# Performance work log

Hardware: AMD Instinct MI355X
Metric: run time of the kernel (lower is better)

## Reference

```python
import jax, jax.numpy as jnp
import numpy as np

IN_F = 4096
OUT_F = 4096
N_VALS = 4096
N_TOKENS = 4096


def setup_inputs() -> dict:
    key = jax.random.key(0)
    k_x, k_v, k_i = jax.random.split(key, 3)
    x = jax.random.normal(k_x, (N_TOKENS, IN_F), dtype=jnp.float32)
    # codebook of memristor conductance differences (sorted, as in load_values)
    values = jnp.sort(jax.random.normal(k_v, (N_VALS,), dtype=jnp.float32))
    w_idx = jax.random.randint(k_i, (OUT_F, IN_F), 0, N_VALS, dtype=jnp.int64)
    bias = jnp.zeros((OUT_F,), dtype=jnp.float32)
    return {"x": x, "values": values, "w_idx": w_idx, "bias": bias}


def reference(x, values, w_idx, bias):
    # dequantize weight from codebook: (out_f, in_f)
    weight = values[w_idx]
    # F.linear(x, weight, bias) == x @ weight.T + bias
    return jnp.einsum("ti,oi->to", x, weight) + bias
```

## Files before the change

### kernel.cpp

```cpp
#include <hip/hip_runtime.h>
#include <hip/hip_bf16.h>
#include <stdint.h>

typedef unsigned short u16;
typedef __bf16 bf16x8 __attribute__((ext_vector_type(8)));
typedef float  f32x4  __attribute__((ext_vector_type(4)));
typedef u16    u16x8  __attribute__((ext_vector_type(8)));
typedef u16    u16x4  __attribute__((ext_vector_type(4)));

__device__ __forceinline__ u16 f2bf(float f) {
  union { float f; unsigned u; } v; v.f = f;
  unsigned u = v.u;
  unsigned r = u + 0x7FFFu + ((u >> 16) & 1u);
  return (u16)(r >> 16);
}

__device__ __forceinline__ void gld_lds16(const void* g, void* l) {
  __builtin_amdgcn_global_load_lds(
      (const __attribute__((address_space(1))) void*)g,
      (__attribute__((address_space(3))) void*)l, 16, 0, 0);
}

__global__ void detect_idx_width(const unsigned* __restrict__ w, int* __restrict__ flag) {
  unsigned v = w[threadIdx.x * 2 + 1];
  unsigned long long any = __ballot(v != 0u);
  if (threadIdx.x == 0) *flag = (any != 0ull) ? 1 : 0;
}

__global__ __launch_bounds__(256) void cvt_x_kernel(const float4* __restrict__ x,
                                                    u16* __restrict__ xb, long n8) {
  long i = (long)blockIdx.x * blockDim.x + threadIdx.x;
  long stride = (long)gridDim.x * blockDim.x;
  for (; i < n8; i += stride) {
    float4 a = x[2 * i];
    float4 b = x[2 * i + 1];
    u16x8 r;
    r[0] = f2bf(a.x); r[1] = f2bf(a.y); r[2] = f2bf(a.z); r[3] = f2bf(a.w);
    r[4] = f2bf(b.x); r[5] = f2bf(b.y); r[6] = f2bf(b.z); r[7] = f2bf(b.w);
    *(u16x8*)(xb + 8 * i) = r;
  }
}

__global__ __launch_bounds__(256) void dequant_w_kernel(const int4* __restrict__ widx,
                                                        const float* __restrict__ values,
                                                        u16* __restrict__ wb,
                                                        const int* __restrict__ flag, long n4) {
  const bool is32 = (*flag != 0);
  long i = (long)blockIdx.x * blockDim.x + threadIdx.x;
  long stride = (long)gridDim.x * blockDim.x;
  for (; i < n4; i += stride) {
    int i0, i1, i2, i3;
    if (is32) {
      int4 v = widx[i];
      i0 = v.x; i1 = v.y; i2 = v.z; i3 = v.w;
    } else {
      int4 a = widx[2 * i];
      int4 b = widx[2 * i + 1];
      i0 = a.x; i1 = a.z; i2 = b.x; i3 = b.z;
    }
    u16x4 r;
    r[0] = f2bf(values[i0]); r[1] = f2bf(values[i1]);
    r[2] = f2bf(values[i2]); r[3] = f2bf(values[i3]);
    *(u16x4*)(wb + 4 * i) = r;
  }
}

#define VMW(n) asm volatile("s_waitcnt vmcnt(" #n ")" ::: "memory")
#define SB0    __builtin_amdgcn_sched_barrier(0)
#define PH_BAR __builtin_amdgcn_s_barrier()

__global__ __launch_bounds__(512, 1) void gemm256_kernel(
    const u16* __restrict__ Xb, const u16* __restrict__ Wb,
    const float* __restrict__ bias, float* __restrict__ C,
    int Nout, int Kin) {
  __shared__ __align__(16) char lds[163840];

  const int tid  = threadIdx.x;
  const int lane = tid & 63;
  const int wave = tid >> 6;
  const int wr = wave >> 2;
  const int wc = wave & 3;

  const int nwg = gridDim.x;
  const int bid = blockIdx.x;
  const int q8 = nwg >> 3, r8 = nwg & 7;
  const int xcd = bid & 7;
  const int wg = (xcd < r8 ? xcd * (q8 + 1) : r8 * (q8 + 1) + (xcd - r8) * q8) + (bid >> 3);

  const int tiles_n = Nout / 256;
  const long brow = (long)(wg / tiles_n) * 256;
  const long bcol = (long)(wg % tiles_n) * 256;

  const long rowb = (long)Kin * 2;
  const long rstep = 64 * rowb;
  const long hstep = 128 * rowb;

  const int f0  = tid * 16;
  const int f1  = f0 + 8192;
  const int rS0 = f0 >> 7;
  const int cS  = (f0 & 127) ^ ((rS0 & 7) << 4);
  const int voff = (int)(rS0 * rowb) + cS;

  const char* uA = (const char*)Xb + (size_t)brow * rowb;
  const char* uB = (const char*)Wb + (size_t)bcol * rowb;

#define STAGE_AH(base_, h, t) { \
  gld_lds16(uA + (size_t)(h) * hstep + (size_t)(t) * 128 + voff,         lds + (base_) + (h) * 16384 + f0); \
  gld_lds16(uA + (size_t)(h) * hstep + (size_t)(t) * 128 + rstep + voff, lds + (base_) + (h) * 16384 + f1); }
#define STAGE_BH(base_, h, t) { \
  gld_lds16(uB + (size_t)(h) * hstep + (size_t)(t) * 128 + voff,         lds + (base_) + (h) * 16384 + f0); \
  gld_lds16(uB + (size_t)(h) * hstep + (size_t)(t) * 128 + rstep + voff, lds + (base_) + (h) * 16384 + f1); }

  const int fr   = lane & 15;
  const int kb   = (lane >> 4) * 16;
  const int xsw  = (fr & 7) << 4;
  const int colx0 = kb ^ xsw;
  const int colx1 = (64 + kb) ^ xsw;
  const int aOff = wr * 16384 + fr * 128;
  const int bOff = (wc >> 1) * 16384 + ((wc & 1) * 64 + fr) * 128;

  bf16x8 afr0[2][2];
  bf16x8 afr1[2][2];
  bf16x8 bfrE[4][2];
  bf16x8 bfrO[4][2];
  f32x4  acc[8][4] = {};

#define READ_AQ(abase_, q, DST) { \
  const char* ab = lds + (abase_) + aOff + (q) * 4096; \
  DST[0][0] = *(const bf16x8*)(ab + colx0); \
  DST[0][1] = *(const bf16x8*)(ab + colx1); \
  DST[1][0] = *(const bf16x8*)(ab + 2048 + colx0); \
  DST[1][1] = *(const bf16x8*)(ab + 2048 + colx1); }

#define READ_BPF(bbase_, dst, lo) { \
  const char* bb = lds + (bbase_) + bOff; \
  dst[(lo)][0]     = *(const bf16x8*)(bb + (lo) * 2048 + colx0); \
  dst[(lo)][1]     = *(const bf16x8*)(bb + (lo) * 2048 + colx1); \
  dst[(lo) + 1][0] = *(const bf16x8*)(bb + ((lo) + 1) * 2048 + colx0); \
  dst[(lo) + 1][1] = *(const bf16x8*)(bb + ((lo) + 1) * 2048 + colx1); }

#define MFMA_Q(q, AF, BF) { \
  __builtin_amdgcn_s_setprio(1); \
  _Pragma("unroll") for (int m2 = 0; m2 < 2; ++m2) \
  _Pragma("unroll") for (int ni = 0; ni < 4; ++ni) { \
    acc[(q)*2+m2][ni] = __builtin_amdgcn_mfma_f32_16x16x32_bf16(AF[m2][0], BF[ni][0], acc[(q)*2+m2][ni], 0, 0, 0); \
    acc[(q)*2+m2][ni] = __builtin_amdgcn_mfma_f32_16x16x32_bf16(AF[m2][1], BF[ni][1], acc[(q)*2+m2][ni], 0, 0, 0); } \
  __builtin_amdgcn_s_setprio(0); }

#define PHASE(RDS, STG, MF, WT) { \
  RDS; STG; SB0; PH_BAR; SB0; MF; SB0; WT; PH_BAR; }

  const int aB0 = 0, aB1 = 32768;
  int bR0 = 65536, bR1 = 98304, bR2 = 131072;
  const int NT = Kin >> 6;

  STAGE_AH(aB0, 0, 0); STAGE_AH(aB0, 1, 0);
  STAGE_BH(bR0, 0, 0); STAGE_BH(bR0, 1, 0);
  if (NT > 1) { STAGE_BH(bR1, 0, 1); STAGE_BH(bR1, 1, 1); }
  if (NT > 2) { STAGE_BH(bR2, 0, 2); STAGE_BH(bR2, 1, 2); }
  VMW(0);
  PH_BAR;
  READ_BPF(bR0, bfrE, 0); READ_BPF(bR0, bfrE, 2);
  READ_AQ(aB0, 0, afr0);

  const int NITER = NT >> 1;
  for (int i = 0; i < NITER; ++i) {
    const int t0 = i * 2;
    const bool a1 = (t0 + 1 < NT);
    const bool a2 = (t0 + 2 < NT);
    const bool b3 = (t0 + 3 < NT);
    const bool b4 = (t0 + 4 < NT);

    PHASE(READ_AQ(aB0, 1, afr1),
          { if (a1) STAGE_AH(aB1, 0, t0 + 1); },
          MFMA_Q(0, afr0, bfrE), (void)0);
    PHASE({ READ_AQ(aB0, 2, afr0); READ_BPF(bR1, bfrO, 0); },
          { if (a1) STAGE_AH(aB1, 1, t0 + 1); },
          MFMA_Q(1, afr1, bfrE), (void)0);
    PHASE({ READ_AQ(aB0, 3, afr1); READ_BPF(bR1, bfrO, 2); },
          { if (b3) STAGE_BH(bR0, 0, t0 + 3); },
          MFMA_Q(2, afr0, bfrE),
          { if (b3) { VMW(2); } else { VMW(0); } });
    PHASE({ if (a1) READ_AQ(aB1, 0, afr0); },
          { if (b3) STAGE_BH(bR0, 1, t0 + 3); },
          MFMA_Q(3, afr1, bfrE), (void)0);

    PHASE(READ_AQ(aB1, 1, afr1),
          { if (a2) STAGE_AH(aB0, 0, t0 + 2); },
          MFMA_Q(0, afr0, bfrO), (void)0);
    PHASE({ READ_AQ(aB1, 2, afr0); if (a2) READ_BPF(bR2, bfrE, 0); },
          { if (a2) STAGE_AH(aB0, 1, t0 + 2); },
          MFMA_Q(1, afr1, bfrO), (void)0);
    PHASE({ READ_AQ(aB1, 3, afr1); if (a2) READ_BPF(bR2, bfrE, 2); },
          { if (b4) STAGE_BH(bR1, 0, t0 + 4); },
          MFMA_Q(2, afr0, bfrO),
          { if (b4) { VMW(2); } else { VMW(0); } });
    PHASE({ if (a2) READ_AQ(aB0, 0, afr0); },
          { if (b4) STAGE_BH(bR1, 1, t0 + 4); },
          MFMA_Q(3, afr1, bfrO), (void)0);

    int tmp = bR0; bR0 = bR2; bR2 = bR1; bR1 = tmp;
  }

  const int cm = (lane >> 4) * 4;
  const int cn = lane & 15;
  float bv[4];
#pragma unroll
  for (int ni = 0; ni < 4; ++ni) bv[ni] = bias[bcol + wc * 64 + ni * 16 + cn];

#pragma unroll
  for (int mi = 0; mi < 8; ++mi) {
    const long row0 = brow + wr * 128 + mi * 16 + cm;
#pragma unroll
    for (int ni = 0; ni < 4; ++ni) {
      const long col = bcol + wc * 64 + ni * 16 + cn;
#pragma unroll
      for (int j = 0; j < 4; ++j)
        C[(row0 + j) * (long)Nout + col] = acc[mi][ni][j] + bv[ni];
    }
  }
#undef STAGE_AH
#undef STAGE_BH
#undef READ_AQ
#undef READ_BPF
#undef MFMA_Q
#undef PHASE
}

__global__ __launch_bounds__(256, 2) void gemm128_kernel(
    const u16* __restrict__ Xb, const u16* __restrict__ Wb,
    const float* __restrict__ bias, float* __restrict__ C,
    int Nout, int Kin) {
  __shared__ __align__(16) u16 As[128 * 32];
  __shared__ __align__(16) u16 Bs[128 * 32];
  const int tid  = threadIdx.x;
  const int lane = tid & 63;
  const int wave = tid >> 6;
  const int wr = wave >> 1, wc = wave & 1;
  const int nwg = gridDim.x, bid = blockIdx.x;
  const int q = nwg >> 3, r8 = nwg & 7;
  const int xcd = bid & 7;
  const int wg = (xcd < r8 ? xcd * (q + 1) : r8 * (q + 1) + (xcd - r8) * q) + (bid >> 3);
  const int tiles_n = Nout / 128;
  const long brow = (long)(wg / tiles_n) * 128;
  const long bcol = (long)(wg % tiles_n) * 128;
  const int f0 = tid * 16, f1 = f0 + 4096;
  const size_t rowbytes = (size_t)Kin * 2;
  const char* gA0 = (const char*)Xb + (size_t)(brow + (f0 >> 6)) * rowbytes + (f0 & 63);
  const char* gA1 = (const char*)Xb + (size_t)(brow + (f1 >> 6)) * rowbytes + (f1 & 63);
  const char* gB0 = (const char*)Wb + (size_t)(bcol + (f0 >> 6)) * rowbytes + (f0 & 63);
  const char* gB1 = (const char*)Wb + (size_t)(bcol + (f1 >> 6)) * rowbytes + (f1 & 63);
  char* lA0 = (char*)As + f0; char* lA1 = (char*)As + f1;
  char* lB0 = (char*)Bs + f0; char* lB1 = (char*)Bs + f1;
  const int fr = lane & 15, kb = (lane >> 4) * 16;
  const char* aptr[4]; const char* bptr[4];
#pragma unroll
  for (int i = 0; i < 4; ++i) {
    aptr[i] = (const char*)As + (wr * 64 + i * 16 + fr) * 64 + kb;
    bptr[i] = (const char*)Bs + (wc * 64 + i * 16 + fr) * 64 + kb;
  }
  f32x4 acc[4][4] = {};
  for (int kk = 0; kk < Kin; kk += 32) {
    const size_t ko = (size_t)kk * 2;
    gld_lds16(gA0 + ko, lA0); gld_lds16(gA1 + ko, lA1);
    gld_lds16(gB0 + ko, lB0); gld_lds16(gB1 + ko, lB1);
    __syncthreads();
    bf16x8 a[4], b[4];
#pragma unroll
    for (int i = 0; i < 4; ++i) a[i] = *(const bf16x8*)aptr[i];
#pragma unroll
    for (int i = 0; i < 4; ++i) b[i] = *(const bf16x8*)bptr[i];
#pragma unroll
    for (int mi = 0; mi < 4; ++mi)
#pragma unroll
      for (int ni = 0; ni < 4; ++ni)
        acc[mi][ni] = __builtin_amdgcn_mfma_f32_16x16x32_bf16(a[mi], b[ni], acc[mi][ni], 0, 0, 0);
    __syncthreads();
  }
  const int cm = (lane >> 4) * 4, cn = lane & 15;
  float bv[4];
#pragma unroll
  for (int ni = 0; ni < 4; ++ni) bv[ni] = bias[bcol + wc * 64 + ni * 16 + cn];
#pragma unroll
  for (int mi = 0; mi < 4; ++mi) {
    const long row0 = brow + wr * 64 + mi * 16 + cm;
#pragma unroll
    for (int ni = 0; ni < 4; ++ni) {
      const long col = bcol + wc * 64 + ni * 16 + cn;
#pragma unroll
      for (int j = 0; j < 4; ++j)
        C[(row0 + j) * (long)Nout + col] = acc[mi][ni][j] + bv[ni];
    }
  }
}

__global__ void fallback_kernel(const float* __restrict__ x, const float* __restrict__ values,
                                const int* __restrict__ widx, const float* __restrict__ bias,
                                float* __restrict__ out, const int* __restrict__ flag,
                                int NT, int IF, int OF) {
  const int o = blockIdx.x * blockDim.x + threadIdx.x;
  const int t = blockIdx.y;
  if (o >= OF || t >= NT) return;
  const bool is32 = (*flag != 0);
  const float* xr = x + (size_t)t * IF;
  float sum = 0.f;
  if (is32) {
    const int* w = widx + (size_t)o * IF;
    for (int k = 0; k < IF; ++k) sum += xr[k] * values[w[k]];
  } else {
    const long long* w = (const long long*)widx + (size_t)o * IF;
    for (int k = 0; k < IF; ++k) sum += xr[k] * values[(int)w[k]];
  }
  out[(size_t)t * OF + o] = sum + bias[o];
}

extern "C" void kernel_launch(void* const* d_in, const int* in_sizes, int n_in,
                              void* d_out, int out_size, void* d_ws, size_t ws_size,
                              hipStream_t stream) {
  const float* x      = (const float*)d_in[0];
  const float* values = (const float*)d_in[1];
  const int*   widx   = (const int*)d_in[2];
  const float* bias   = (const float*)d_in[3];
  float* out = (float*)d_out;

  const long xsz = in_sizes[0];
  const int  OF  = in_sizes[3];
  const long wsz = in_sizes[2];
  const int  IF  = (int)(wsz / OF);
  const int  NTOK = (int)(xsz / IF);

  u16* xb = (u16*)d_ws;
  u16* wb = xb + (size_t)NTOK * IF;
  int* flag = (int*)(wb + (size_t)OF * IF);
  const size_t need = ((size_t)NTOK * IF + (size_t)OF * IF) * sizeof(u16) + 64;

  const bool pre_ok = (ws_size >= need) && ((xsz % 8) == 0) && ((wsz % 4) == 0);
  const bool f256 = pre_ok && (IF % 128 == 0) && (IF >= 256) &&
                    (NTOK % 256 == 0) && (OF % 256 == 0);
  const bool f128 = pre_ok && (IF % 32 == 0) && (NTOK % 128 == 0) && (OF % 128 == 0);

  if (f256 || f128) {
    hipLaunchKernelGGL(detect_idx_width, dim3(1), dim3(64), 0, stream,
                       (const unsigned*)widx, flag);
    hipLaunchKernelGGL(cvt_x_kernel, dim3(2048), dim3(256), 0, stream,
                       (const float4*)x, xb, xsz / 8);
    hipLaunchKernelGGL(dequant_w_kernel, dim3(2048), dim3(256), 0, stream,
                       (const int4*)widx, values, wb, (const int*)flag, wsz / 4);
    if (f256) {
      const int grid = (NTOK / 256) * (OF / 256);
      hipLaunchKernelGGL(gemm256_kernel, dim3(grid), dim3(512), 0, stream,
                         xb, wb, bias, out, OF, IF);
    } else {
      const int grid = (NTOK / 128) * (OF / 128);
      hipLaunchKernelGGL(gemm128_kernel, dim3(grid), dim3(256), 0, stream,
                         xb, wb, bias, out, OF, IF);
    }
  } else {
    int* flag2 = (int*)d_ws;
    hipLaunchKernelGGL(detect_idx_width, dim3(1), dim3(64), 0, stream,
                       (const unsigned*)widx, flag2);
    hipLaunchKernelGGL(fallback_kernel, dim3((OF + 255) / 256, NTOK), dim3(256), 0, stream,
                       x, values, widx, bias, out, (const int*)flag2, NTOK, IF, OF);
  }
}
```

Baseline: 170.2 us.

## Restructure GEMM main-loop phases: drop extra sched barriers, move vmcnt waits later

Removes two of the three sched_barrier fences inside each phase, which lets the compiler interleave LDS reads, global-to-LDS stages and MFMAs more freely. A-fragment reads move so each tile's first two quarter-fragments load at its first phase instead of being prefetched in the previous tile's last phase. The global-load wait moves from phase 3 to phase 4 with a looser vmcnt (4 instead of 2). This is meant to give memory more overlap with compute and cut stalls, at the cost of losing the A-fragment prefetch across tiles and relying on the compiler's own scheduling.

```diff
diff --git a/kernel.cpp b/kernel.cpp
--- a/kernel.cpp
+++ b/kernel.cpp
@@ -119,8 +119,8 @@
   const int aOff = wr * 16384 + fr * 128;
   const int bOff = (wc >> 1) * 16384 + ((wc & 1) * 64 + fr) * 128;
 
-  bf16x8 afr0[2][2];
-  bf16x8 afr1[2][2];
+  bf16x8 afrA[2][2];
+  bf16x8 afrB[2][2];
   bf16x8 bfrE[4][2];
   bf16x8 bfrO[4][2];
   f32x4  acc[8][4] = {};
@@ -148,7 +148,7 @@
   __builtin_amdgcn_s_setprio(0); }
 
 #define PHASE(RDS, STG, MF, WT) { \
-  RDS; STG; SB0; PH_BAR; SB0; MF; SB0; WT; PH_BAR; }
+  RDS; STG; SB0; PH_BAR; MF; WT; PH_BAR; }
 
   const int aB0 = 0, aB1 = 32768;
   int bR0 = 65536, bR1 = 98304, bR2 = 131072;
@@ -161,7 +161,6 @@
   VMW(0);
   PH_BAR;
   READ_BPF(bR0, bfrE, 0); READ_BPF(bR0, bfrE, 2);
-  READ_AQ(aB0, 0, afr0);
 
   const int NITER = NT >> 1;
   for (int i = 0; i < NITER; ++i) {
@@ -171,33 +170,33 @@
     const bool b3 = (t0 + 3 < NT);
     const bool b4 = (t0 + 4 < NT);
 
-    PHASE(READ_AQ(aB0, 1, afr1),
+    PHASE({ READ_AQ(aB0, 0, afrA); READ_AQ(aB0, 1, afrB); },
           { if (a1) STAGE_AH(aB1, 0, t0 + 1); },
-          MFMA_Q(0, afr0, bfrE), (void)0);
-    PHASE({ READ_AQ(aB0, 2, afr0); READ_BPF(bR1, bfrO, 0); },
+          MFMA_Q(0, afrA, bfrE), (void)0);
+    PHASE({ READ_AQ(aB0, 2, afrA); if (a1) READ_BPF(bR1, bfrO, 0); },
           { if (a1) STAGE_AH(aB1, 1, t0 + 1); },
-          MFMA_Q(1, afr1, bfrE), (void)0);
-    PHASE({ READ_AQ(aB0, 3, afr1); READ_BPF(bR1, bfrO, 2); },
+          MFMA_Q(1, afrB, bfrE), (void)0);
+    PHASE({ READ_AQ(aB0, 3, afrB); if (a1) READ_BPF(bR1, bfrO, 2); },
           { if (b3) STAGE_BH(bR0, 0, t0 + 3); },
-          MFMA_Q(2, afr0, bfrE),
-          { if (b3) { VMW(2); } else { VMW(0); } });
-    PHASE({ if (a1) READ_AQ(aB1, 0, afr0); },
+          MFMA_Q(2, afrA, bfrE), (void)0);
+    PHASE({ (void)0; },
           { if (b3) STAGE_BH(bR0, 1, t0 + 3); },
-          MFMA_Q(3, afr1, bfrE), (void)0);
-
-    PHASE(READ_AQ(aB1, 1, afr1),
+          MFMA_Q(3, afrB, bfrE),
+          { if (b3) { VMW(4); } else { VMW(0); } });
+
+    PHASE({ READ_AQ(aB1, 0, afrA); READ_AQ(aB1, 1, afrB); },
           { if (a2) STAGE_AH(aB0, 0, t0 + 2); },
-          MFMA_Q(0, afr0, bfrO), (void)0);
-    PHASE({ READ_AQ(aB1, 2, afr0); if (a2) READ_BPF(bR2, bfrE, 0); },
+          MFMA_Q(0, afrA, bfrO), (void)0);
+    PHASE({ READ_AQ(aB1, 2, afrA); if (a2) READ_BPF(bR2, bfrE, 0); },
           { if (a2) STAGE_AH(aB0, 1, t0 + 2); },
-          MFMA_Q(1, afr1, bfrO), (void)0);
-    PHASE({ READ_AQ(aB1, 3, afr1); if (a2) READ_BPF(bR2, bfrE, 2); },
+          MFMA_Q(1, afrB, bfrO), (void)0);
+    PHASE({ READ_AQ(aB1, 3, afrB); if (a2) READ_BPF(bR2, bfrE, 2); },
           { if (b4) STAGE_BH(bR1, 0, t0 + 4); },
-          MFMA_Q(2, afr0, bfrO),
-          { if (b4) { VMW(2); } else { VMW(0); } });
-    PHASE({ if (a2) READ_AQ(aB0, 0, afr0); },
+          MFMA_Q(2, afrA, bfrO), (void)0);
+    PHASE({ (void)0; },
           { if (b4) STAGE_BH(bR1, 1, t0 + 4); },
-          MFMA_Q(3, afr1, bfrO), (void)0);
+          MFMA_Q(3, afrB, bfrO),
+          { if (b4) { VMW(4); } else { VMW(0); } });
 
     int tmp = bR0; bR0 = bR2; bR2 = bR1; bR1 = tmp;
   }
```

After: 170.3 us. No clear change (+0.1%).
